# Kernel optimization log

Hardware: AMD Instinct MI355X
Metric: run time of the kernel (lower is better)

## Reference

```python
import jax, jax.numpy as jnp
import numpy as np

EPS = 1e-6
GROUPS = 32


def group_norm(x, scale, bias):
    # x: [b, c, d, h, w]
    b, c, d, h, w = x.shape
    xg = x.reshape(b, GROUPS, c // GROUPS, d, h, w)
    mean = xg.mean(axis=(2, 3, 4, 5), keepdims=True)
    var = xg.var(axis=(2, 3, 4, 5), keepdims=True)
    xn = ((xg - mean) * jax.lax.rsqrt(var + EPS)).reshape(b, c, d, h, w)
    return xn * scale[None, :, None, None, None] + bias[None, :, None, None, None]


def setup_inputs() -> dict:
    key = jax.random.key(0)
    ks = jax.random.split(key, 6)
    C = 512
    x = jax.random.normal(ks[0], (2, C, 16, 16, 16), dtype=jnp.float32)
    s = 1.0 / np.sqrt(C)
    return {
        "x": x,
        "gn_scale": jnp.ones((C,), jnp.float32),
        "gn_bias": jnp.zeros((C,), jnp.float32),
        "wq": jax.random.normal(ks[1], (C, C), jnp.float32) * s,
        "bq": jnp.zeros((C,), jnp.float32),
        "wk": jax.random.normal(ks[2], (C, C), jnp.float32) * s,
        "bk": jnp.zeros((C,), jnp.float32),
        "wv": jax.random.normal(ks[3], (C, C), jnp.float32) * s,
        "bv": jnp.zeros((C,), jnp.float32),
        "wproj": jax.random.normal(ks[4], (C, C), jnp.float32) * s,
        "bproj": jnp.zeros((C,), jnp.float32),
    }


def reference(x, gn_scale, gn_bias, wq, bq, wk, bk, wv, bv, wproj, bproj):
    b, c, d, h, w = x.shape
    h_ = group_norm(x, gn_scale, gn_bias)
    hf = h_.reshape(b, c, d * h * w)  # [b, c, N]
    # 1x1x1 convs == per-position channel matmuls
    q = jnp.einsum("oc,bcn->bon", wq, hf) + bq[None, :, None]
    k = jnp.einsum("oc,bcn->bon", wk, hf) + bk[None, :, None]
    v = jnp.einsum("oc,bcn->bon", wv, hf) + bv[None, :, None]
    # attn[b, i, j] = softmax_j(q_i . k_j / sqrt(c))
    attn = jnp.einsum("bci,bcj->bij", q, k) * (c ** -0.5)
    attn = jax.nn.softmax(attn, axis=-1)
    # out[b, c, i] = sum_j v[b, c, j] * attn[b, i, j]
    out = jnp.einsum("bcj,bij->bci", v, attn)
    out = jnp.einsum("oc,bcn->bon", wproj, out) + bproj[None, :, None]
    return x + out.reshape(b, c, d, h, w)
```

## Files before the change

kernel.cpp:

```cpp
#include <hip/hip_runtime.h>
#include <hip/hip_bf16.h>

#define BB 2
#define CC 512
#define GG 32
#define NN 4096
#define EPSV 1e-6f

typedef __attribute__((ext_vector_type(4))) float f32x4;
typedef __attribute__((ext_vector_type(8))) short s16x8;
typedef __attribute__((ext_vector_type(4))) short s16x4;

__device__ __forceinline__ ushort f2bf(float f){
  union { float f; unsigned u; } v; v.f = f;
  unsigned r = v.u + 0x7fffu + ((v.u >> 16) & 1u);
  return (ushort)(r >> 16);
}
__device__ __forceinline__ short f2bfs(float f){ return (short)f2bf(f); }
__device__ __forceinline__ float b2f(ushort u){
  union { unsigned u; float f; } v; v.u = ((unsigned)u) << 16; return v.f;
}

__device__ __forceinline__ f32x4 mfma16(s16x8 a, s16x8 b, f32x4 c){
  return __builtin_amdgcn_mfma_f32_16x16x32_bf16(a, b, c, 0, 0, 0);
}

#define GLOAD_LDS16(g, l) __builtin_amdgcn_global_load_lds( \
    (const __attribute__((address_space(1))) void*)(g),     \
    (__attribute__((address_space(3))) void*)(l), 16, 0, 0)

__global__ __launch_bounds__(256) void k_convert_w(const float* __restrict__ wq, const float* __restrict__ wk,
                                                   const float* __restrict__ wv, const float* __restrict__ wp,
                                                   ushort* __restrict__ wbf){
  int idx = blockIdx.x * 256 + threadIdx.x;
  const float* srcs[4] = {wq, wk, wv, wp};
  #pragma unroll
  for (int m = 0; m < 4; m++){
    float4 v = reinterpret_cast<const float4*>(srcs[m])[idx];
    ushort4 o; o.x = f2bf(v.x); o.y = f2bf(v.y); o.z = f2bf(v.z); o.w = f2bf(v.w);
    reinterpret_cast<ushort4*>(wbf + (size_t)m * CC * CC)[idx] = o;
  }
}

__global__ __launch_bounds__(256) void k_gn_stats(const float* __restrict__ x, float* __restrict__ stats){
  int bg = blockIdx.x;
  const float* p = x + (size_t)bg * (16 * NN);
  float s = 0.f, ss = 0.f;
  for (int i = threadIdx.x; i < 16 * NN / 4; i += 256){
    float4 v = reinterpret_cast<const float4*>(p)[i];
    s  += v.x + v.y + v.z + v.w;
    ss += v.x*v.x + v.y*v.y + v.z*v.z + v.w*v.w;
  }
  #pragma unroll
  for (int off = 32; off; off >>= 1){ s += __shfl_down(s, off); ss += __shfl_down(ss, off); }
  __shared__ float rs_[4], rss_[4];
  int w = threadIdx.x >> 6, lane = threadIdx.x & 63;
  if (lane == 0){ rs_[w] = s; rss_[w] = ss; }
  __syncthreads();
  if (threadIdx.x == 0){
    float S = rs_[0] + rs_[1] + rs_[2] + rs_[3];
    float SS = rss_[0] + rss_[1] + rss_[2] + rss_[3];
    float inv = 1.0f / (16.0f * NN);
    float mean = S * inv;
    float var = SS * inv - mean * mean;
    stats[bg * 2 + 0] = mean;
    stats[bg * 2 + 1] = rsqrtf(var + EPSV);
  }
}

__global__ __launch_bounds__(256) void k_gn_apply(const float* __restrict__ x, const float* __restrict__ gsc,
                                                  const float* __restrict__ gbi, const float* __restrict__ stats,
                                                  ushort* __restrict__ hf){
  __shared__ ushort tr[32][520];
  int b = blockIdx.y;
  int nb = blockIdx.x * 32;
  int t = threadIdx.x;
  int n = t & 31, cr = t >> 5;
  const float* xb = x + (size_t)b * CC * NN;
  for (int c0 = 0; c0 < CC; c0 += 8){
    int c = c0 + cr;
    float mean = stats[(b * GG + (c >> 4)) * 2 + 0];
    float rstd = stats[(b * GG + (c >> 4)) * 2 + 1];
    float v = xb[(size_t)c * NN + nb + n];
    tr[n][c] = f2bf((v - mean) * rstd * gsc[c] + gbi[c]);
  }
  __syncthreads();
  ushort* out = hf + ((size_t)b * NN + nb) * CC;
  int c8 = (t & 63) * 8;
  int nrow0 = t >> 6;
  #pragma unroll
  for (int i = 0; i < 8; i++){
    int nr = nrow0 + i * 4;
    *reinterpret_cast<s16x8*>(&out[(size_t)nr * CC + c8]) =
      *reinterpret_cast<const s16x8*>(&tr[nr][c8]);
  }
}

__global__ __launch_bounds__(256, 3) void k_gemm_qkv2(const ushort* __restrict__ W, const ushort* __restrict__ Bt,
                                                      const float* __restrict__ bq, const float* __restrict__ bk,
                                                      const float* __restrict__ bv,
                                                      ushort* __restrict__ qo, ushort* __restrict__ ko,
                                                      ushort* __restrict__ vo, float rs){
  __shared__ __align__(16) char smem[40960];
  __shared__ float bl[3][64];
  int b = blockIdx.z, ob = blockIdx.y * 64, nb = blockIdx.x * 128;
  int t = threadIdx.x, w = t >> 6, l = t & 63;
  int lr = l & 15, lk = l >> 4;
  int wo = (w >> 1) * 32, wn = (w & 1) * 64;
  if (t < 64){ bl[0][t] = bq[ob + t]; bl[1][t] = bk[ob + t]; bl[2][t] = bv[ob + t]; }
  const ushort* Bp = Bt + ((size_t)b * NN + nb) * CC;
  const ushort* Wp = W + (size_t)ob * CC;
  int srow = l >> 2;
  int schunk = (l & 3) ^ ((l >> 2) & 3) ^ ((l >> 4) & 3);
  int xs = (lk ^ (lr & 3) ^ ((lr >> 2) & 3)) * 8;

#define STAGE_QKV(BUF, K0)                                                               \
  {                                                                                      \
    ushort* As_ = (ushort*)(smem + (BUF) * 20480);                                       \
    ushort* Bs_ = As_ + 6144;                                                            \
    _Pragma("unroll")                                                                    \
    for (int tt = 0; tt < 5; tt++){                                                      \
      int inst = w * 5 + tt;                                                             \
      if (inst < 12){                                                                    \
        int m = inst >> 2, sub = inst & 3;                                               \
        const ushort* src = Wp + (size_t)m * CC * CC + (size_t)(sub * 16 + srow) * CC + (K0) + schunk * 8; \
        GLOAD_LDS16(src, As_ + m * 2048 + sub * 512);                                    \
      } else {                                                                           \
        int q = inst - 12;                                                               \
        const ushort* src = Bp + (size_t)(q * 16 + srow) * CC + (K0) + schunk * 8;       \
        GLOAD_LDS16(src, Bs_ + q * 512);                                                 \
      }                                                                                  \
    }                                                                                    \
  }

  f32x4 acc[3][2][4] = {};
  STAGE_QKV(0, 0)
  __syncthreads();
  for (int s16 = 0; s16 < 16; s16++){
    if (s16 < 15) STAGE_QKV((s16 + 1) & 1, (s16 + 1) * 32)
    const ushort* As = (const ushort*)(smem + (s16 & 1) * 20480);
    const ushort* Bs = As + 6144;
    s16x8 bf[4];
    #pragma unroll
    for (int sn = 0; sn < 4; sn++)
      bf[sn] = *(const s16x8*)&Bs[(wn + sn * 16 + lr) * 32 + xs];
    #pragma unroll
    for (int m = 0; m < 3; m++){
      s16x8 a0 = *(const s16x8*)&As[m * 2048 + (wo + lr) * 32 + xs];
      s16x8 a1 = *(const s16x8*)&As[m * 2048 + (wo + 16 + lr) * 32 + xs];
      #pragma unroll
      for (int sn = 0; sn < 4; sn++){
        acc[m][0][sn] = mfma16(a0, bf[sn], acc[m][0][sn]);
        acc[m][1][sn] = mfma16(a1, bf[sn], acc[m][1][sn]);
      }
    }
    __syncthreads();
  }
#undef STAGE_QKV
  #pragma unroll
  for (int m = 0; m < 2; m++){
    ushort* dst = (m == 0) ? qo : ko;
    float scl = (m == 0) ? rs : 1.0f;
    #pragma unroll
    for (int so = 0; so < 2; so++)
      #pragma unroll
      for (int sn = 0; sn < 4; sn++){
        int o0 = wo + so * 16 + lk * 4;
        int n  = nb + wn + sn * 16 + lr;
        s16x4 pv;
        #pragma unroll
        for (int r = 0; r < 4; r++) pv[r] = f2bfs((acc[m][so][sn][r] + bl[m][o0 + r]) * scl);
        *reinterpret_cast<s16x4*>(&dst[((size_t)b * NN + n) * CC + ob + o0]) = pv;
      }
  }
  ushort* Ve = (ushort*)smem;
  #pragma unroll
  for (int so = 0; so < 2; so++)
    #pragma unroll
    for (int sn = 0; sn < 4; sn++){
      int o0 = wo + so * 16 + lk * 4;
      int ncl = wn + sn * 16 + lr;
      #pragma unroll
      for (int r = 0; r < 4; r++) Ve[(o0 + r) * 136 + ncl] = f2bf(acc[2][so][sn][r] + bl[2][o0 + r]);
    }
  __syncthreads();
  {
    int row = t >> 2, cs = (t & 3) * 32;
    ushort* dst = &vo[((size_t)b * CC + ob + row) * NN + nb + cs];
    #pragma unroll
    for (int k = 0; k < 4; k++)
      *(s16x8*)&dst[k * 8] = *(const s16x8*)&Ve[row * 136 + cs + k * 8];
  }
}

__global__ __launch_bounds__(256) void k_gemm_s(const ushort* __restrict__ qt, const ushort* __restrict__ kt,
                                                ushort* __restrict__ P, float* __restrict__ part){
  __shared__ __align__(16) char smem[65536];
  int lin = blockIdx.x + 32 * blockIdx.y + 1024 * blockIdx.z;
  int tt0 = (lin & 7) * 256 + (lin >> 3);
  int jblk = tt0 & 31;
  int pair = tt0 >> 5;
  int b = pair >> 5;
  int j0 = jblk * 128, i0 = (pair & 31) * 128;
  int t = threadIdx.x, w = t >> 6, l = t & 63;
  int lr = l & 15, lk = l >> 4;
  int wj = (w >> 1) * 64, wi = (w & 1) * 64;
  const ushort* kb = kt + ((size_t)b * NN + j0) * CC;
  const ushort* qb = qt + ((size_t)b * NN + i0) * CC;
  int srow = l >> 3;
  int schunk = (l & 7) ^ srow;

#define STAGE_S(BUF, K0)                                                          \
  {                                                                               \
    ushort* Ks_ = (ushort*)(smem + (BUF) * 16384);                                \
    ushort* Qs_ = (ushort*)(smem + 32768 + (BUF) * 16384);                        \
    _Pragma("unroll")                                                             \
    for (int tt = 0; tt < 8; tt++){                                               \
      int inst = w * 8 + tt;                                                      \
      if (inst < 16){                                                             \
        const ushort* src = kb + (size_t)(inst * 8 + srow) * CC + (K0) + schunk * 8; \
        GLOAD_LDS16(src, Ks_ + inst * 512);                                       \
      } else {                                                                    \
        int q = inst - 16;                                                        \
        const ushort* src = qb + (size_t)(q * 8 + srow) * CC + (K0) + schunk * 8; \
        GLOAD_LDS16(src, Qs_ + q * 512);                                          \
      }                                                                           \
    }                                                                             \
  }

  f32x4 acc[4][4] = {};
  STAGE_S(0, 0)
  __syncthreads();
  for (int s8 = 0; s8 < 8; s8++){
    if (s8 < 7) STAGE_S((s8 + 1) & 1, (s8 + 1) * 64)
    const ushort* Ks = (const ushort*)(smem + (s8 & 1) * 16384);
    const ushort* Qs = (const ushort*)(smem + 32768 + (s8 & 1) * 16384);
    #pragma unroll
    for (int kk = 0; kk < 2; kk++){
      int xs = ((kk * 4 + lk) ^ (lr & 7)) * 8;
      s16x8 af[4], bf[4];
      #pragma unroll
      for (int s = 0; s < 4; s++){
        af[s] = *(const s16x8*)&Ks[(wj + s * 16 + lr) * 64 + xs];
        bf[s] = *(const s16x8*)&Qs[(wi + s * 16 + lr) * 64 + xs];
      }
      #pragma unroll
      for (int sj = 0; sj < 4; sj++)
        #pragma unroll
        for (int si = 0; si < 4; si++)
          acc[sj][si] = mfma16(af[sj], bf[si], acc[sj][si]);
    }
    __syncthreads();
  }
#undef STAGE_S
  ushort* Pe = (ushort*)smem;
  float rsum[4] = {0.f, 0.f, 0.f, 0.f};
  #pragma unroll
  for (int sj = 0; sj < 4; sj++)
    #pragma unroll
    for (int si = 0; si < 4; si++){
      int il = wi + si * 16 + lr;
      int jl = wj + sj * 16 + lk * 4;
      s16x4 pk;
      #pragma unroll
      for (int r = 0; r < 4; r++){
        float e = __builtin_amdgcn_exp2f(acc[sj][si][r]);
        pk[r] = f2bfs(e);
        rsum[si] += e;
      }
      *(s16x4*)&Pe[il * 136 + jl] = pk;
    }
  #pragma unroll
  for (int si = 0; si < 4; si++){
    float s = rsum[si];
    s += __shfl_xor(s, 16);
    s += __shfl_xor(s, 32);
    if (lk == 0){
      int il = wi + si * 16 + lr;
      part[((size_t)b * NN + i0 + il) * 64 + jblk * 2 + (w >> 1)] = s;
    }
  }
  __syncthreads();
  {
    int row = t >> 1, cs = (t & 1) * 64;
    ushort* dst = P + ((size_t)b * NN + i0 + row) * NN + j0 + cs;
    #pragma unroll
    for (int k = 0; k < 8; k++)
      *(s16x8*)&dst[k * 8] = *(const s16x8*)&Pe[row * 136 + cs + k * 8];
  }
}

__global__ __launch_bounds__(256) void k_rowsum2(const float* __restrict__ part, float* __restrict__ linv){
  int row = blockIdx.x * 4 + (threadIdx.x >> 6);
  int l = threadIdx.x & 63;
  float s = part[(size_t)row * 64 + l];
  #pragma unroll
  for (int off = 32; off; off >>= 1) s += __shfl_down(s, off);
  if (l == 0) linv[row] = 1.0f / s;
}

__global__ __launch_bounds__(512) void k_gemm_o(const ushort* __restrict__ P, const ushort* __restrict__ vv,
                                                const float* __restrict__ linv, ushort* __restrict__ ot){
  __shared__ __align__(16) char smem[49152];
  int lin = blockIdx.x + 8 * blockIdx.y + 256 * blockIdx.z;
  int tt0 = (lin & 7) * 64 + (lin >> 3);
  int cblk = tt0 & 7;
  int pair = tt0 >> 3;
  int b = pair >> 5;
  int c0 = cblk * 64, i0 = (pair & 31) * 128;
  int t = threadIdx.x, w = t >> 6, l = t & 63;
  int lr = l & 15, lk = l >> 4;
  int wi = (w >> 1) * 32, wc = (w & 1) * 32;
  const ushort* vb = vv + ((size_t)b * CC + c0) * NN;
  const ushort* pb = P + ((size_t)b * NN + i0) * NN;
  int srow = l >> 3;
  int schunk = (l & 7) ^ srow;

#define STAGE_O(BUF, K0)                                                          \
  {                                                                               \
    ushort* Vs_ = (ushort*)(smem + (BUF) * 8192);                                 \
    ushort* Ps_ = (ushort*)(smem + 16384 + (BUF) * 16384);                        \
    _Pragma("unroll")                                                             \
    for (int tt = 0; tt < 3; tt++){                                               \
      int inst = w * 3 + tt;                                                      \
      if (inst < 8){                                                              \
        const ushort* src = vb + (size_t)(inst * 8 + srow) * NN + (K0) + schunk * 8; \
        GLOAD_LDS16(src, Vs_ + inst * 512);                                       \
      } else {                                                                    \
        int q = inst - 8;                                                         \
        const ushort* src = pb + (size_t)(q * 8 + srow) * NN + (K0) + schunk * 8; \
        GLOAD_LDS16(src, Ps_ + q * 512);                                          \
      }                                                                           \
    }                                                                             \
  }

  f32x4 acc[2][2] = {};
  STAGE_O(0, 0)
  __syncthreads();
  for (int s64 = 0; s64 < 64; s64++){
    if (s64 < 63) STAGE_O((s64 + 1) & 1, (s64 + 1) * 64)
    const ushort* Vs = (const ushort*)(smem + (s64 & 1) * 8192);
    const ushort* Ps = (const ushort*)(smem + 16384 + (s64 & 1) * 16384);
    #pragma unroll
    for (int kk = 0; kk < 2; kk++){
      int xs = ((kk * 4 + lk) ^ (lr & 7)) * 8;
      s16x8 af[2], bf[2];
      af[0] = *(const s16x8*)&Vs[(wc + lr) * 64 + xs];
      af[1] = *(const s16x8*)&Vs[(wc + 16 + lr) * 64 + xs];
      bf[0] = *(const s16x8*)&Ps[(wi + lr) * 64 + xs];
      bf[1] = *(const s16x8*)&Ps[(wi + 16 + lr) * 64 + xs];
      acc[0][0] = mfma16(af[0], bf[0], acc[0][0]);
      acc[0][1] = mfma16(af[0], bf[1], acc[0][1]);
      acc[1][0] = mfma16(af[1], bf[0], acc[1][0]);
      acc[1][1] = mfma16(af[1], bf[1], acc[1][1]);
    }
    __syncthreads();
  }
#undef STAGE_O
  ushort* Oe = (ushort*)smem;
  #pragma unroll
  for (int si = 0; si < 2; si++){
    int il = wi + si * 16 + lr;
    float li = linv[(size_t)b * NN + i0 + il];
    #pragma unroll
    for (int sc = 0; sc < 2; sc++){
      int cl = wc + sc * 16 + lk * 4;
      s16x4 pk;
      #pragma unroll
      for (int r = 0; r < 4; r++) pk[r] = f2bfs(acc[sc][si][r] * li);
      *(s16x4*)&Oe[il * 72 + cl] = pk;
    }
  }
  __syncthreads();
  {
    int row = t >> 2, cs = (t & 3) * 16;
    ushort* dst = ot + ((size_t)b * NN + i0 + row) * CC + c0 + cs;
    #pragma unroll
    for (int k = 0; k < 2; k++)
      *(s16x8*)&dst[k * 8] = *(const s16x8*)&Oe[row * 72 + cs + k * 8];
  }
}

__global__ __launch_bounds__(256, 3) void k_gemm_proj2(const ushort* __restrict__ A, const ushort* __restrict__ Bt,
                                                       const float* __restrict__ bias, float* __restrict__ o32,
                                                       const float* __restrict__ xres){
  __shared__ __align__(16) char smem[34048];
  __shared__ float bl[64];
  int b = blockIdx.z, ob = blockIdx.y * 64, nb = blockIdx.x * 128;
  int t = threadIdx.x, w = t >> 6, l = t & 63;
  int lr = l & 15, lk = l >> 4;
  int wo = (w >> 1) * 32, wn = (w & 1) * 64;
  if (t < 64) bl[t] = bias[ob + t];
  const ushort* Bp = Bt + ((size_t)b * NN + nb) * CC;
  const ushort* Ap = A + (size_t)ob * CC;
  int srow = l >> 2;
  int schunk = (l & 3) ^ ((l >> 2) & 3) ^ ((l >> 4) & 3);
  int xs = (lk ^ (lr & 3) ^ ((lr >> 2) & 3)) * 8;

#define STAGE_P2(BUF, K0)                                                         \
  {                                                                               \
    ushort* As_ = (ushort*)(smem + (BUF) * 12288);                                \
    ushort* Bs_ = As_ + 2048;                                                     \
    _Pragma("unroll")                                                             \
    for (int tt = 0; tt < 3; tt++){                                               \
      int inst = w * 3 + tt;                                                      \
      if (inst < 4){                                                              \
        const ushort* src = Ap + (size_t)(inst * 16 + srow) * CC + (K0) + schunk * 8; \
        GLOAD_LDS16(src, As_ + inst * 512);                                       \
      } else {                                                                    \
        int q = inst - 4;                                                         \
        const ushort* src = Bp + (size_t)(q * 16 + srow) * CC + (K0) + schunk * 8; \
        GLOAD_LDS16(src, Bs_ + q * 512);                                          \
      }                                                                           \
    }                                                                             \
  }

  f32x4 acc[2][4] = {};
  STAGE_P2(0, 0)
  __syncthreads();
  for (int s16 = 0; s16 < 16; s16++){
    if (s16 < 15) STAGE_P2((s16 + 1) & 1, (s16 + 1) * 32)
    const ushort* As = (const ushort*)(smem + (s16 & 1) * 12288);
    const ushort* Bs = As + 2048;
    s16x8 a0 = *(const s16x8*)&As[(wo + lr) * 32 + xs];
    s16x8 a1 = *(const s16x8*)&As[(wo + 16 + lr) * 32 + xs];
    #pragma unroll
    for (int sn = 0; sn < 4; sn++){
      s16x8 bf = *(const s16x8*)&Bs[(wn + sn * 16 + lr) * 32 + xs];
      acc[0][sn] = mfma16(a0, bf, acc[0][sn]);
      acc[1][sn] = mfma16(a1, bf, acc[1][sn]);
    }
    __syncthreads();
  }
#undef STAGE_P2
  float* trf = (float*)smem;
  #pragma unroll
  for (int so = 0; so < 2; so++)
    #pragma unroll
    for (int sn = 0; sn < 4; sn++){
      int o0 = wo + so * 16 + lk * 4;
      int ncl = wn + sn * 16 + lr;
      #pragma unroll
      for (int r = 0; r < 4; r++) trf[(o0 + r) * 133 + ncl] = acc[so][sn][r] + bl[o0 + r];
    }
  __syncthreads();
  {
    int row = t >> 2, cs = (t & 3) * 32;
    size_t base = ((size_t)b * CC + ob + row) * NN + nb + cs;
    #pragma unroll
    for (int q = 0; q < 8; q++){
      float4 xv = *reinterpret_cast<const float4*>(&xres[base + q * 4]);
      float4 ov;
      ov.x = xv.x + trf[row * 133 + cs + q * 4 + 0];
      ov.y = xv.y + trf[row * 133 + cs + q * 4 + 1];
      ov.z = xv.z + trf[row * 133 + cs + q * 4 + 2];
      ov.w = xv.w + trf[row * 133 + cs + q * 4 + 3];
      *reinterpret_cast<float4*>(&o32[base + q * 4]) = ov;
    }
  }
}

extern "C" void kernel_launch(void* const* d_in, const int* in_sizes, int n_in,
                              void* d_out, int out_size, void* d_ws, size_t ws_size,
                              hipStream_t stream){
  const float* x   = (const float*)d_in[0];
  const float* gsc = (const float*)d_in[1];
  const float* gbi = (const float*)d_in[2];
  const float* wq  = (const float*)d_in[3];
  const float* bq  = (const float*)d_in[4];
  const float* wk  = (const float*)d_in[5];
  const float* bk  = (const float*)d_in[6];
  const float* wv  = (const float*)d_in[7];
  const float* bv  = (const float*)d_in[8];
  const float* wp  = (const float*)d_in[9];
  const float* bp  = (const float*)d_in[10];
  char* ws = (char*)d_ws;
  const size_t MB = 1024 * 1024;
  ushort* wbf  = (ushort*)ws;
  ushort* qtb  = (ushort*)(ws + 2 * MB);
  ushort* ktb  = (ushort*)(ws + 10 * MB);
  ushort* vvb  = (ushort*)(ws + 18 * MB);
  ushort* hfb  = (ushort*)(ws + 26 * MB);
  ushort* Pbuf = (ushort*)(ws + 34 * MB);
  float* linv  = (float*)(ws + 98 * MB);
  float* stats = (float*)(ws + 98 * MB + 64 * 1024);
  float* part  = (float*)(ws + 26 * MB);
  ushort* otb = hfb;

  const float rs = 0.044194173824159216f * 1.4426950408889634f;

  k_convert_w<<<256, 256, 0, stream>>>(wq, wk, wv, wp, wbf);
  k_gn_stats<<<64, 256, 0, stream>>>(x, stats);
  k_gn_apply<<<dim3(128, 2, 1), 256, 0, stream>>>(x, gsc, gbi, stats, hfb);
  k_gemm_qkv2<<<dim3(32, 8, 2), 256, 0, stream>>>(wbf, hfb, bq, bk, bv, qtb, ktb, vvb, rs);
  k_gemm_s<<<dim3(32, 32, 2), 256, 0, stream>>>(qtb, ktb, Pbuf, part);
  k_rowsum2<<<2048, 256, 0, stream>>>(part, linv);
  k_gemm_o<<<dim3(8, 32, 2), 512, 0, stream>>>(Pbuf, vvb, linv, otb);
  k_gemm_proj2<<<dim3(32, 8, 2), 256, 0, stream>>>(wbf + 3 * CC * CC, otb, bp, (float*)d_out, x);
}
```

Measured before the change: 192.2 us.

## Load Q fragments directly to registers in score GEMM, shrink LDS for occupancy

The score GEMM kernel stops staging Q tiles through shared memory and reads Q MFMA fragments straight from global memory into registers, prefetching the next half-K slice while the current one is consumed. Only K is double-buffered in LDS, so the allocation shrinks and launch bounds request 3 blocks per CU. The aim is to cut LDS traffic and raise occupancy. The cost is uncoalesced, row-strided global loads for Q that depend on cache hits, plus possible register pressure from the tighter launch bound.

Result: slower. 213.7 us (+11.2%).

```diff
diff --git a/kernel.cpp b/kernel.cpp
--- a/kernel.cpp
+++ b/kernel.cpp
@@ -193,9 +193,9 @@
   }
 }
 
-__global__ __launch_bounds__(256) void k_gemm_s(const ushort* __restrict__ qt, const ushort* __restrict__ kt,
-                                                ushort* __restrict__ P, float* __restrict__ part){
-  __shared__ __align__(16) char smem[65536];
+__global__ __launch_bounds__(256, 3) void k_gemm_s(const ushort* __restrict__ qt, const ushort* __restrict__ kt,
+                                                   ushort* __restrict__ P, float* __restrict__ part){
+  __shared__ __align__(16) char smem[35840];
   int lin = blockIdx.x + 32 * blockIdx.y + 1024 * blockIdx.z;
   int tt0 = (lin & 7) * 256 + (lin >> 3);
   int jblk = tt0 & 31;
@@ -210,49 +210,59 @@
   int srow = l >> 3;
   int schunk = (l & 7) ^ srow;
 
-#define STAGE_S(BUF, K0)                                                          \
+#define STAGE_K(BUF, K0)                                                          \
   {                                                                               \
     ushort* Ks_ = (ushort*)(smem + (BUF) * 16384);                                \
-    ushort* Qs_ = (ushort*)(smem + 32768 + (BUF) * 16384);                        \
     _Pragma("unroll")                                                             \
-    for (int tt = 0; tt < 8; tt++){                                               \
-      int inst = w * 8 + tt;                                                      \
-      if (inst < 16){                                                             \
-        const ushort* src = kb + (size_t)(inst * 8 + srow) * CC + (K0) + schunk * 8; \
-        GLOAD_LDS16(src, Ks_ + inst * 512);                                       \
-      } else {                                                                    \
-        int q = inst - 16;                                                        \
-        const ushort* src = qb + (size_t)(q * 8 + srow) * CC + (K0) + schunk * 8; \
-        GLOAD_LDS16(src, Qs_ + q * 512);                                          \
-      }                                                                           \
+    for (int tt = 0; tt < 4; tt++){                                               \
+      int inst = w * 4 + tt;                                                      \
+      const ushort* src = kb + (size_t)(inst * 8 + srow) * CC + (K0) + schunk * 8; \
+      GLOAD_LDS16(src, Ks_ + inst * 512);                                         \
     }                                                                             \
   }
+#define QFRAG(SI, K0, KK) \
+  (*(const s16x8*)&qb[(size_t)(wi + (SI) * 16 + lr) * CC + (K0) + ((KK) * 4 + lk) * 8])
 
   f32x4 acc[4][4] = {};
-  STAGE_S(0, 0)
+  STAGE_K(0, 0)
+  s16x8 bq0[4], bq1[4];
+  #pragma unroll
+  for (int si = 0; si < 4; si++) bq0[si] = QFRAG(si, 0, 0);
   __syncthreads();
   for (int s8 = 0; s8 < 8; s8++){
-    if (s8 < 7) STAGE_S((s8 + 1) & 1, (s8 + 1) * 64)
+    int k0 = s8 * 64;
+    if (s8 < 7) STAGE_K((s8 + 1) & 1, k0 + 64)
     const ushort* Ks = (const ushort*)(smem + (s8 & 1) * 16384);
-    const ushort* Qs = (const ushort*)(smem + 32768 + (s8 & 1) * 16384);
-    #pragma unroll
-    for (int kk = 0; kk < 2; kk++){
-      int xs = ((kk * 4 + lk) ^ (lr & 7)) * 8;
-      s16x8 af[4], bf[4];
-      #pragma unroll
-      for (int s = 0; s < 4; s++){
-        af[s] = *(const s16x8*)&Ks[(wj + s * 16 + lr) * 64 + xs];
-        bf[s] = *(const s16x8*)&Qs[(wi + s * 16 + lr) * 64 + xs];
-      }
-      #pragma unroll
-      for (int sj = 0; sj < 4; sj++)
+    #pragma unroll
+    for (int si = 0; si < 4; si++) bq1[si] = QFRAG(si, k0, 1);
+    {
+      int xs = (lk ^ (lr & 7)) * 8;
+      #pragma unroll
+      for (int sj = 0; sj < 4; sj++){
+        s16x8 a = *(const s16x8*)&Ks[(wj + sj * 16 + lr) * 64 + xs];
         #pragma unroll
         for (int si = 0; si < 4; si++)
-          acc[sj][si] = mfma16(af[sj], bf[si], acc[sj][si]);
+          acc[sj][si] = mfma16(a, bq0[si], acc[sj][si]);
+      }
+    }
+    if (s8 < 7){
+      #pragma unroll
+      for (int si = 0; si < 4; si++) bq0[si] = QFRAG(si, k0 + 64, 0);
+    }
+    {
+      int xs = ((4 + lk) ^ (lr & 7)) * 8;
+      #pragma unroll
+      for (int sj = 0; sj < 4; sj++){
+        s16x8 a = *(const s16x8*)&Ks[(wj + sj * 16 + lr) * 64 + xs];
+        #pragma unroll
+        for (int si = 0; si < 4; si++)
+          acc[sj][si] = mfma16(a, bq1[si], acc[sj][si]);
+      }
     }
     __syncthreads();
   }
-#undef STAGE_S
+#undef STAGE_K
+#undef QFRAG
   ushort* Pe = (ushort*)smem;
   float rsum[4] = {0.f, 0.f, 0.f, 0.f};
   #pragma unroll
```

## Enlarge QK^T score tile to 256x256 with 512-thread blocks

Applied to the files above, without the earlier changes.

The score GEMM/exp kernel moves from 128x128 tiles with 256 threads to 256x256 tiles with 512 threads, backed by 128KB of dynamic LDS. Each wave now computes a 128x64 sub-tile, reusing its Q fragments across eight K fragments. The P write-out is split into two passes over 128 rows so the staging buffer fits in LDS. The per-row partial sums shrink from 64 to 32 entries, and the rowsum kernel is adjusted to match. Larger tiles cut redundant global loads of Q and K, at the cost of fewer blocks, lower occupancy and extra barriers in the epilogue.

After: 188.7 us. Within noise of the previous version (-1.8%).

```diff
diff --git a/kernel.cpp b/kernel.cpp
--- a/kernel.cpp
+++ b/kernel.cpp
@@ -193,18 +193,18 @@
   }
 }
 
-__global__ __launch_bounds__(256) void k_gemm_s(const ushort* __restrict__ qt, const ushort* __restrict__ kt,
-                                                ushort* __restrict__ P, float* __restrict__ part){
-  __shared__ __align__(16) char smem[65536];
-  int lin = blockIdx.x + 32 * blockIdx.y + 1024 * blockIdx.z;
-  int tt0 = (lin & 7) * 256 + (lin >> 3);
-  int jblk = tt0 & 31;
-  int pair = tt0 >> 5;
-  int b = pair >> 5;
-  int j0 = jblk * 128, i0 = (pair & 31) * 128;
+__global__ __launch_bounds__(512, 2) void k_gemm_s(const ushort* __restrict__ qt, const ushort* __restrict__ kt,
+                                                   ushort* __restrict__ P, float* __restrict__ part){
+  extern __shared__ __align__(16) char smem[];
+  int lin = blockIdx.x + 16 * blockIdx.y + 256 * blockIdx.z;
+  int tt0 = (lin & 7) * 64 + (lin >> 3);
+  int jblk = tt0 & 15;
+  int pair = tt0 >> 4;
+  int b = pair >> 4;
+  int j0 = jblk * 256, i0 = (pair & 15) * 256;
   int t = threadIdx.x, w = t >> 6, l = t & 63;
   int lr = l & 15, lk = l >> 4;
-  int wj = (w >> 1) * 64, wi = (w & 1) * 64;
+  int wj2 = w >> 2, wi4 = w & 3;
   const ushort* kb = kt + ((size_t)b * NN + j0) * CC;
   const ushort* qb = qt + ((size_t)b * NN + i0) * CC;
   int srow = l >> 3;
@@ -212,43 +212,43 @@
 
 #define STAGE_S(BUF, K0)                                                          \
   {                                                                               \
-    ushort* Ks_ = (ushort*)(smem + (BUF) * 16384);                                \
-    ushort* Qs_ = (ushort*)(smem + 32768 + (BUF) * 16384);                        \
+    ushort* Ks_ = (ushort*)(smem + (BUF) * 32768);                                \
+    ushort* Qs_ = (ushort*)(smem + 65536 + (BUF) * 32768);                        \
     _Pragma("unroll")                                                             \
     for (int tt = 0; tt < 8; tt++){                                               \
       int inst = w * 8 + tt;                                                      \
-      if (inst < 16){                                                             \
+      if (inst < 32){                                                             \
         const ushort* src = kb + (size_t)(inst * 8 + srow) * CC + (K0) + schunk * 8; \
         GLOAD_LDS16(src, Ks_ + inst * 512);                                       \
       } else {                                                                    \
-        int q = inst - 16;                                                        \
-        const ushort* src = qb + (size_t)(q * 8 + srow) * CC + (K0) + schunk * 8; \
-        GLOAD_LDS16(src, Qs_ + q * 512);                                          \
+        int g = inst - 32;                                                        \
+        const ushort* src = qb + (size_t)(g * 8 + srow) * CC + (K0) + schunk * 8; \
+        GLOAD_LDS16(src, Qs_ + g * 512);                                          \
       }                                                                           \
     }                                                                             \
   }
 
-  f32x4 acc[4][4] = {};
+  f32x4 acc[8][4] = {};
   STAGE_S(0, 0)
   __syncthreads();
   for (int s8 = 0; s8 < 8; s8++){
     if (s8 < 7) STAGE_S((s8 + 1) & 1, (s8 + 1) * 64)
-    const ushort* Ks = (const ushort*)(smem + (s8 & 1) * 16384);
-    const ushort* Qs = (const ushort*)(smem + 32768 + (s8 & 1) * 16384);
+    const ushort* Ks = (const ushort*)(smem + (s8 & 1) * 32768);
+    const ushort* Qs = (const ushort*)(smem + 65536 + (s8 & 1) * 32768);
     #pragma unroll
     for (int kk = 0; kk < 2; kk++){
       int xs = ((kk * 4 + lk) ^ (lr & 7)) * 8;
-      s16x8 af[4], bf[4];
-      #pragma unroll
-      for (int s = 0; s < 4; s++){
-        af[s] = *(const s16x8*)&Ks[(wj + s * 16 + lr) * 64 + xs];
-        bf[s] = *(const s16x8*)&Qs[(wi + s * 16 + lr) * 64 + xs];
-      }
-      #pragma unroll
-      for (int sj = 0; sj < 4; sj++)
+      s16x8 bf[4];
+      #pragma unroll
+      for (int si = 0; si < 4; si++)
+        bf[si] = *(const s16x8*)&Qs[(wi4 * 64 + si * 16 + lr) * 64 + xs];
+      #pragma unroll
+      for (int sj = 0; sj < 8; sj++){
+        s16x8 a = *(const s16x8*)&Ks[(wj2 * 128 + sj * 16 + lr) * 64 + xs];
         #pragma unroll
         for (int si = 0; si < 4; si++)
-          acc[sj][si] = mfma16(af[sj], bf[si], acc[sj][si]);
+          acc[sj][si] = mfma16(a, bf[si], acc[sj][si]);
+      }
     }
     __syncthreads();
   }
@@ -256,44 +256,50 @@
   ushort* Pe = (ushort*)smem;
   float rsum[4] = {0.f, 0.f, 0.f, 0.f};
   #pragma unroll
-  for (int sj = 0; sj < 4; sj++)
-    #pragma unroll
-    for (int si = 0; si < 4; si++){
-      int il = wi + si * 16 + lr;
-      int jl = wj + sj * 16 + lk * 4;
-      s16x4 pk;
-      #pragma unroll
-      for (int r = 0; r < 4; r++){
-        float e = __builtin_amdgcn_exp2f(acc[sj][si][r]);
-        pk[r] = f2bfs(e);
-        rsum[si] += e;
-      }
-      *(s16x4*)&Pe[il * 136 + jl] = pk;
-    }
+  for (int pass = 0; pass < 2; pass++){
+    if ((wi4 >> 1) == pass){
+      #pragma unroll
+      for (int sj = 0; sj < 8; sj++)
+        #pragma unroll
+        for (int si = 0; si < 4; si++){
+          int il = (wi4 & 1) * 64 + si * 16 + lr;
+          int jl = wj2 * 128 + sj * 16 + lk * 4;
+          s16x4 pk;
+          #pragma unroll
+          for (int r = 0; r < 4; r++){
+            float e = __builtin_amdgcn_exp2f(acc[sj][si][r]);
+            pk[r] = f2bfs(e);
+            rsum[si] += e;
+          }
+          *(s16x4*)&Pe[il * 264 + jl] = pk;
+        }
+    }
+    __syncthreads();
+    {
+      int row = t >> 2, cs = (t & 3) * 64;
+      ushort* dst = P + ((size_t)b * NN + i0 + pass * 128 + row) * NN + j0 + cs;
+      #pragma unroll
+      for (int k = 0; k < 8; k++)
+        *(s16x8*)&dst[k * 8] = *(const s16x8*)&Pe[row * 264 + cs + k * 8];
+    }
+    __syncthreads();
+  }
   #pragma unroll
   for (int si = 0; si < 4; si++){
     float s = rsum[si];
     s += __shfl_xor(s, 16);
     s += __shfl_xor(s, 32);
     if (lk == 0){
-      int il = wi + si * 16 + lr;
-      part[((size_t)b * NN + i0 + il) * 64 + jblk * 2 + (w >> 1)] = s;
-    }
-  }
-  __syncthreads();
-  {
-    int row = t >> 1, cs = (t & 1) * 64;
-    ushort* dst = P + ((size_t)b * NN + i0 + row) * NN + j0 + cs;
-    #pragma unroll
-    for (int k = 0; k < 8; k++)
-      *(s16x8*)&dst[k * 8] = *(const s16x8*)&Pe[row * 136 + cs + k * 8];
+      int il = wi4 * 64 + si * 16 + lr;
+      part[((size_t)b * NN + i0 + il) * 32 + jblk * 2 + wj2] = s;
+    }
   }
 }
 
 __global__ __launch_bounds__(256) void k_rowsum2(const float* __restrict__ part, float* __restrict__ linv){
   int row = blockIdx.x * 4 + (threadIdx.x >> 6);
   int l = threadIdx.x & 63;
-  float s = part[(size_t)row * 64 + l];
+  float s = (l < 32) ? part[(size_t)row * 32 + l] : 0.f;
   #pragma unroll
   for (int off = 32; off; off >>= 1) s += __shfl_down(s, off);
   if (l == 0) linv[row] = 1.0f / s;
@@ -493,7 +499,7 @@
   k_gn_stats<<<64, 256, 0, stream>>>(x, stats);
   k_gn_apply<<<dim3(128, 2, 1), 256, 0, stream>>>(x, gsc, gbi, stats, hfb);
   k_gemm_qkv2<<<dim3(32, 8, 2), 256, 0, stream>>>(wbf, hfb, bq, bk, bv, qtb, ktb, vvb, rs);
-  k_gemm_s<<<dim3(32, 32, 2), 256, 0, stream>>>(qtb, ktb, Pbuf, part);
+  k_gemm_s<<<dim3(16, 16, 2), 512, 131072, stream>>>(qtb, ktb, Pbuf, part);
   k_rowsum2<<<2048, 256, 0, stream>>>(part, linv);
   k_gemm_o<<<dim3(8, 32, 2), 512, 0, stream>>>(Pbuf, vvb, linv, otb);
   k_gemm_proj2<<<dim3(32, 8, 2), 256, 0, stream>>>(wbf + 3 * CC * CC, otb, bp, (float*)d_out, x);
```
